# Kernel optimization log

Measured on AMD Instinct MI355X. Metric: run time of the kernel, lower is better.

Reference implementation:

```python
import jax, jax.numpy as jnp
import numpy as np
import math

B, S, D_IN, D_OUT = 2, 2048, 2048, 2048
N_HEADS, N_KV = 32, 8
HEAD_DIM = D_OUT // N_HEADS  # 64
GROUP = N_HEADS // N_KV      # 4


def _rope_tables(seq_len, head_dim, base=10000.0):
    inv_freq = 1.0 / (base ** (jnp.arange(0, head_dim, 2, dtype=jnp.float32) / head_dim))
    angles = jnp.arange(seq_len, dtype=jnp.float32)[:, None] * inv_freq[None, :]  # [S, hd/2]
    angles = jnp.concatenate([angles, angles], axis=-1)  # [S, hd]
    return jnp.cos(angles), jnp.sin(angles)


def setup_inputs() -> dict:
    key = jax.random.key(0)
    kx, kq, kk, kv, ko = jax.random.split(key, 5)
    x = jax.random.normal(kx, (B, S, D_IN), dtype=jnp.float32)
    # causal mask: True where attention is disallowed (j > i)
    mask = jnp.triu(jnp.ones((S, S), dtype=bool), k=1)
    cos, sin = _rope_tables(S, HEAD_DIM)
    scale = 0.02
    Wq = jax.random.normal(kq, (D_IN, D_OUT), dtype=jnp.float32) * scale
    Wk = jax.random.normal(kk, (D_IN, N_KV * HEAD_DIM), dtype=jnp.float32) * scale
    Wv = jax.random.normal(kv, (D_IN, N_KV * HEAD_DIM), dtype=jnp.float32) * scale
    Wo = jax.random.normal(ko, (D_OUT, D_OUT), dtype=jnp.float32) * scale
    return {"x": x, "mask": mask, "cos": cos, "sin": sin,
            "Wq": Wq, "Wk": Wk, "Wv": Wv, "Wo": Wo}


def _apply_rope(t, cos, sin):
    # t: [B, H, S, hd]; cos/sin: [S, hd]
    hd = t.shape[-1]
    t1, t2 = t[..., : hd // 2], t[..., hd // 2:]
    rotated = jnp.concatenate([-t2, t1], axis=-1)
    return t * cos[None, None] + rotated * sin[None, None]


def reference(x, mask, cos, sin, Wq, Wk, Wv, Wo):
    b, s, _ = x.shape
    q = (x @ Wq).reshape(b, s, N_HEADS, HEAD_DIM).transpose(0, 2, 1, 3)  # [B,H,S,hd]
    k = (x @ Wk).reshape(b, s, N_KV, HEAD_DIM).transpose(0, 2, 1, 3)    # [B,G,S,hd]
    v = (x @ Wv).reshape(b, s, N_KV, HEAD_DIM).transpose(0, 2, 1, 3)
    q = _apply_rope(q, cos, sin)
    k = _apply_rope(k, cos, sin)
    # repeat_interleave KV heads to match query heads
    k = jnp.repeat(k, GROUP, axis=1)  # [B,H,S,hd]
    v = jnp.repeat(v, GROUP, axis=1)
    scores = jnp.einsum('bhqd,bhkd->bhqk', q, k)
    scores = jnp.where(mask[None, None], -1e9, scores)
    weights = jax.nn.softmax(scores / math.sqrt(HEAD_DIM), axis=-1)
    ctx = jnp.einsum('bhqk,bhkd->bhqd', weights, v)
    ctx = ctx.transpose(0, 2, 1, 3).reshape(b, s, D_OUT)
    return ctx @ Wo
```

## Files before the change

kernel.cpp:

```cpp
#include <hip/hip_runtime.h>
#include <hip/hip_bf16.h>

using bf16 = __bf16;
using bf16x8 = __attribute__((ext_vector_type(8))) __bf16;
using bf16x4 = __attribute__((ext_vector_type(4))) __bf16;
using f32x4  = __attribute__((ext_vector_type(4))) float;
using f32x16 = __attribute__((ext_vector_type(16))) float;

typedef const void __attribute__((address_space(1)))* gas_p;
typedef void __attribute__((address_space(3)))* las_p;

#define GLD16(g, l) __builtin_amdgcn_global_load_lds((gas_p)(const void*)(g), (las_p)(void*)(l), 16, 0, 0)

__device__ __forceinline__ bf16x8 lds_ld8(const void* p) {
  union { uint4 u; bf16x8 v; } c;
  c.u = *(const uint4*)p;
  return c.v;
}
__device__ __forceinline__ bf16x8 g_ld8(const bf16* p) {
  union { uint4 u; bf16x8 v; } c;
  c.u = *(const uint4*)p;
  return c.v;
}
__device__ __forceinline__ float fexp2(float x) {
  float r; asm("v_exp_f32 %0, %1" : "=v"(r) : "v"(x)); return r;
}
__device__ __forceinline__ unsigned cvtpk(float lo, float hi) {
  unsigned r; asm("v_cvt_pk_bf16_f32 %0, %1, %2" : "=v"(r) : "v"(lo), "v"(hi)); return r;
}

__global__ void k_pre(const float* __restrict__ x, bf16* __restrict__ xb,
                      const float* __restrict__ Wq, const float* __restrict__ Wk,
                      const float* __restrict__ Wv, const float* __restrict__ Wo,
                      bf16* __restrict__ wqkv, bf16* __restrict__ wo_t) {
  const int id = blockIdx.x;
  if (id < 8192) {
    const int i = id * 256 + threadIdx.x;
    float4 f = ((const float4*)x)[i];
    bf16x4 o;
    o[0] = (bf16)f.x; o[1] = (bf16)f.y; o[2] = (bf16)f.z; o[3] = (bf16)f.w;
    ((bf16x4*)xb)[i] = o;
    return;
  }
  __shared__ float tile[64][65];
  const int u0 = id - 8192;
  const float* W; bf16* dst; int N, rowOff, bx, by;
  if (u0 < 1024)      { W = Wq; dst = wqkv; N = 2048; rowOff = 0;    bx = u0 & 31; by = u0 >> 5; }
  else if (u0 < 1280) { int u = u0 - 1024; W = Wk; dst = wqkv; N = 512; rowOff = 2048; bx = u & 7; by = u >> 3; }
  else if (u0 < 1536) { int u = u0 - 1280; W = Wv; dst = wqkv; N = 512; rowOff = 2560; bx = u & 7; by = u >> 3; }
  else                { int u = u0 - 1536; W = Wo; dst = wo_t; N = 2048; rowOff = 0;   bx = u & 31; by = u >> 5; }
  const int n0 = bx * 64, k0 = by * 64;
  const int t = threadIdx.x;
#pragma unroll
  for (int i = 0; i < 16; ++i) {
    int idx = t + i * 256; int r = idx >> 6, c = idx & 63;
    tile[r][c] = W[(size_t)(k0 + r) * N + n0 + c];
  }
  __syncthreads();
#pragma unroll
  for (int i = 0; i < 16; ++i) {
    int idx = t + i * 256; int r = idx >> 6, c = idx & 63;
    dst[(size_t)(rowOff + n0 + r) * 2048 + k0 + c] = (bf16)tile[c][r];
  }
}

__device__ __forceinline__ void gemm_main(const bf16* __restrict__ A, const bf16* __restrict__ Bt,
                                          int brow, int bcol, int tid, f32x4 (&acc)[4][4],
                                          char* ldsA, char* ldsB) {
  const int lane = tid & 63;
  const int l15 = lane & 15, l4 = lane >> 4;
  const int wid = tid >> 6, wr = wid >> 1, wc = wid & 1;
  const int srow = tid >> 3;
  const int xseg = (tid & 7) ^ (srow & 7);
  const bf16* ga = A  + (size_t)(brow + srow) * 2048 + xseg * 8;
  const bf16* gb = Bt + (size_t)(bcol + srow) * 2048 + xseg * 8;
  char* la = ldsA + tid * 16;
  char* lb = ldsB + tid * 16;

  for (int k0 = 0; k0 < 2048; k0 += 64) {
    __syncthreads();
#pragma unroll
    for (int i = 0; i < 4; ++i) {
      GLD16(ga + k0 + (size_t)(32 * i) * 2048, la + i * 4096);
      GLD16(gb + k0 + (size_t)(32 * i) * 2048, lb + i * 4096);
    }
    __syncthreads();
#pragma unroll
    for (int kk = 0; kk < 2; ++kk) {
      bf16x8 af[4], bfr[4];
#pragma unroll
      for (int m = 0; m < 4; ++m) {
        const int row = wr * 64 + m * 16 + l15;
        af[m] = lds_ld8(ldsA + row * 128 + ((kk * 64 + l4 * 16) ^ ((row & 7) << 4)));
      }
#pragma unroll
      for (int n = 0; n < 4; ++n) {
        const int row = wc * 64 + n * 16 + l15;
        bfr[n] = lds_ld8(ldsB + row * 128 + ((kk * 64 + l4 * 16) ^ ((row & 7) << 4)));
      }
#pragma unroll
      for (int m = 0; m < 4; ++m)
#pragma unroll
        for (int n = 0; n < 4; ++n)
          acc[m][n] = __builtin_amdgcn_mfma_f32_16x16x32_bf16(af[m], bfr[n], acc[m][n], 0, 0, 0);
    }
  }
}

__global__ __launch_bounds__(256) void k_gemm_qkv(const bf16* __restrict__ A, const bf16* __restrict__ Bt,
    const float* __restrict__ cosT, const float* __restrict__ sinT,
    bf16* __restrict__ Qb, bf16* __restrict__ Kb, bf16* __restrict__ Vt) {
  __shared__ __align__(16) char ldsA[16384];
  __shared__ __align__(16) char ldsB[16384];
  const int tid = threadIdx.x;
  const int p = (int)blockIdx.x, r8 = p & 7, q8 = p >> 3;
  const int by = r8 * 3 + q8 % 3, bx = q8 / 3;
  const int brow = bx * 128, bcol = by * 128;
  f32x4 zero = {0.f, 0.f, 0.f, 0.f};
  f32x4 acc[4][4];
#pragma unroll
  for (int m = 0; m < 4; ++m)
#pragma unroll
    for (int n = 0; n < 4; ++n) acc[m][n] = zero;

  gemm_main(A, Bt, brow, bcol, tid, acc, ldsA, ldsB);

  const int lane = tid & 63, l15 = lane & 15, l4 = lane >> 4;
  const int wid = tid >> 6, wr = wid >> 1, wc = wid & 1;
  const int base64 = bcol + wc * 64;
  const int rbase  = brow + wr * 64;

  if (base64 < 2048) {
    const int h = base64 >> 6;
#pragma unroll
    for (int m = 0; m < 4; ++m)
#pragma unroll
      for (int r = 0; r < 4; ++r) {
        const int row = rbase + m * 16 + l4 * 4 + r;
        const int b = row >> 11, s = row & 2047;
        float o[4];
#pragma unroll
        for (int n = 0; n < 4; ++n) {
          const int d = n * 16 + l15;
          const float cv = cosT[s * 64 + d], sv = sinT[s * 64 + d];
          const float t = acc[m][n][r], pp = acc[m][n ^ 2][r];
          o[n] = (t * cv + ((n < 2) ? -pp : pp) * sv) * 0.18033688f;
        }
        bf16* dst = Qb + ((size_t)((b * 32 + h) * 2048 + s)) * 64;
#pragma unroll
        for (int n = 0; n < 4; ++n) dst[n * 16 + l15] = (bf16)o[n];
      }
  } else if (base64 < 2560) {
    const int h = (base64 - 2048) >> 6;
#pragma unroll
    for (int m = 0; m < 4; ++m)
#pragma unroll
      for (int r = 0; r < 4; ++r) {
        const int row = rbase + m * 16 + l4 * 4 + r;
        const int b = row >> 11, s = row & 2047;
        float o[4];
#pragma unroll
        for (int n = 0; n < 4; ++n) {
          const int d = n * 16 + l15;
          const float cv = cosT[s * 64 + d], sv = sinT[s * 64 + d];
          const float t = acc[m][n][r], pp = acc[m][n ^ 2][r];
          o[n] = t * cv + ((n < 2) ? -pp : pp) * sv;
        }
        bf16* dst = Kb + ((size_t)((b * 8 + h) * 2048 + s)) * 64;
#pragma unroll
        for (int n = 0; n < 4; ++n) dst[n * 16 + l15] = (bf16)o[n];
      }
  } else {
    const int h = (base64 - 2560) >> 6;
#pragma unroll
    for (int m = 0; m < 4; ++m)
#pragma unroll
      for (int r = 0; r < 4; ++r) {
        const int row = rbase + m * 16 + l4 * 4 + r;
        const int b = row >> 11, s = row & 2047;
        const int ps = (s & ~12) | ((s & 4) << 1) | ((s & 8) >> 1);
#pragma unroll
        for (int n = 0; n < 4; ++n) {
          const int d = n * 16 + l15;
          Vt[((size_t)((b * 8 + h) * 64 + d)) * 2048 + ps] = (bf16)acc[m][n][r];
        }
      }
  }
}

__global__ __launch_bounds__(256) void k_attn(const bf16* __restrict__ Qb, const bf16* __restrict__ Kb,
                                              const bf16* __restrict__ Vtp, bf16* __restrict__ ctx) {
  __shared__ __align__(16) char kvb[3][16384];
  __shared__ __align__(16) char tbuf[4][4096];
  const int tid = threadIdx.x, lane = tid & 63, w = tid >> 6;
  const int l31 = lane & 31, hi = lane >> 5;
  const int p = (int)blockIdx.x;
  const int y = (p & 7) * 8 + ((p >> 3) & 7);
  const int j = p >> 6;
  const int b = y >> 5, h = y & 31, hk = h >> 2;
  int c = 15 - j;
  const int ntA = 2 * c + 2;
  const int NT = 34;
  int q0 = c * 128 + w * 32;
  int nf = (q0 + 31) >> 6;

  const int srow = tid >> 3, sseg = tid & 7;
  const bf16* kS = Kb  + ((size_t)((b * 8 + hk) * 2048)) * 64;
  const bf16* vS = Vtp + ((size_t)((b * 8 + hk) * 64)) * 2048;
  const int sz = (l31 & 7) << 4;
  const int wsz = (srow & 7) << 4;

  const f32x16 z16 = {0,0,0,0,0,0,0,0,0,0,0,0,0,0,0,0};
  f32x16 o[2];
  float m, lsum;
  bf16x8 bq[4];

  auto load_q = [&]() {
    const bf16* qbase = Qb + ((size_t)((b * 32 + h) * 2048 + q0 + l31)) * 64 + hi * 8;
#pragma unroll
    for (int dc = 0; dc < 4; ++dc) bq[dc] = g_ld8(qbase + dc * 16);
  };
  load_q();
  o[0] = z16; o[1] = z16; m = -3.0e38f; lsum = 0.f;

  uint4 st[4];
  auto stage_load = [&](int kv0) {
#pragma unroll
    for (int r4 = 0; r4 < 4; ++r4) {
      const int row = srow + (r4 & 1) * 32;
      const bf16* g = (r4 < 2) ? (kS + (size_t)(kv0 + row) * 64 + sseg * 8)
                               : (vS + (size_t)row * 2048 + kv0 + sseg * 8);
      st[r4] = *(const uint4*)g;
    }
  };
  auto stage_write = [&](char* buf) {
#pragma unroll
    for (int r4 = 0; r4 < 4; ++r4)
      *(uint4*)(buf + (srow + r4 * 32) * 128 + ((sseg * 16) ^ wsz)) = st[r4];
  };

  union PF { unsigned u[4]; bf16x8 v; };
  PF pf[4];
  int pend = 0, pslot = 0;

  auto pv_issue = [&](char* pbuf) {
    __builtin_amdgcn_s_setprio(1);
#pragma unroll
    for (int cc = 0; cc < 4; ++cc)
#pragma unroll
      for (int dh = 0; dh < 2; ++dh) {
        const int row = 64 + dh * 32 + l31;
        bf16x8 av = lds_ld8(pbuf + row * 128 + ((cc * 32 + hi * 16) ^ sz));
        o[dh] = __builtin_amdgcn_mfma_f32_32x32x16_bf16(av, pf[cc].v, o[dh], 0, 0, 0);
      }
    __builtin_amdgcn_s_setprio(0);
  };

  auto epilogue = [&]() {
    float ll = lsum + __shfl_xor(lsum, 32);
    const float inv = 1.0f / ll;
    char* tb = tbuf[w];
#pragma unroll
    for (int dh = 0; dh < 2; ++dh)
#pragma unroll
      for (int r = 0; r < 16; r += 2) {
        const unsigned wdv = cvtpk(o[dh][r] * inv, o[dh][r + 1] * inv);
        const int d = dh * 32 + (r & 3) + 8 * (r >> 2) + 4 * hi;
        *(unsigned*)(tb + l31 * 128 + ((d * 2) ^ sz)) = wdv;
      }
#pragma unroll
    for (int jj = 0; jj < 4; ++jj) {
      const int off = hi * 16 + jj * 32;
      uint4 val = *(const uint4*)(tb + l31 * 128 + (off ^ sz));
      *(uint4*)(ctx + ((size_t)(b * 2048 + q0 + l31)) * 2048 + h * 64 + off / 2) = val;
    }
  };

  stage_load(0);
  stage_write(kvb[0]);
  __syncthreads();

  for (int g = 0; g < NT; ++g) {
    const int kt = (g < ntA) ? g : g - ntA;
    char* cur = kvb[g % 3];
    if (g + 1 < NT) {
      const int gn = g + 1;
      stage_load(((gn < ntA) ? gn : gn - ntA) * 64);
    }
    if (pend) { pv_issue(kvb[pslot]); pend = 0; }
    if (kt <= nf) {
      const int kv0 = kt * 64;
      f32x16 sc[2];
      __builtin_amdgcn_s_setprio(1);
#pragma unroll
      for (int kvh = 0; kvh < 2; ++kvh) {
        const int row = kvh * 32 + l31;
        bf16x8 a0 = lds_ld8(cur + row * 128 + ((hi * 16) ^ sz));
        sc[kvh] = __builtin_amdgcn_mfma_f32_32x32x16_bf16(a0, bq[0], z16, 0, 0, 0);
#pragma unroll
        for (int dc = 1; dc < 4; ++dc) {
          bf16x8 ad = lds_ld8(cur + row * 128 + ((dc * 32 + hi * 16) ^ sz));
          sc[kvh] = __builtin_amdgcn_mfma_f32_32x32x16_bf16(ad, bq[dc], sc[kvh], 0, 0, 0);
        }
      }
      __builtin_amdgcn_s_setprio(0);
      if (kt == nf) {
        const int q = q0 + l31;
#pragma unroll
        for (int kvh = 0; kvh < 2; ++kvh)
#pragma unroll
          for (int r = 0; r < 16; ++r) {
            const int kv = kv0 + kvh * 32 + (r & 3) + 8 * (r >> 2) + 4 * hi;
            if (kv > q) sc[kvh][r] = -3.0e30f;
          }
      }
      float t[16];
#pragma unroll
      for (int i = 0; i < 16; ++i) t[i] = fmaxf(sc[0][i], sc[1][i]);
#pragma unroll
      for (int stp = 8; stp >= 1; stp >>= 1)
#pragma unroll
        for (int i = 0; i < stp; ++i) t[i] = fmaxf(t[i], t[i + stp]);
      float mx = fmaxf(t[0], __shfl_xor(t[0], 32));
      if (!__all(mx <= m + 11.5f)) {
        const float mn = fmaxf(m, mx);
        const float corr = fexp2(m - mn);
        m = mn;
        lsum *= corr;
#pragma unroll
        for (int r = 0; r < 16; ++r) { o[0][r] *= corr; o[1][r] *= corr; }
      }
#pragma unroll
      for (int kvh = 0; kvh < 2; ++kvh)
#pragma unroll
        for (int r = 0; r < 16; ++r) sc[kvh][r] = fexp2(sc[kvh][r] - m);
#pragma unroll
      for (int kvh = 0; kvh < 2; ++kvh)
#pragma unroll
        for (int s = 0; s < 2; ++s)
#pragma unroll
          for (int tt = 0; tt < 4; ++tt)
            pf[kvh * 2 + s].u[tt] = cvtpk(sc[kvh][s * 8 + 2 * tt], sc[kvh][s * 8 + 2 * tt + 1]);
      pend = 1; pslot = g % 3;
      float u[16];
#pragma unroll
      for (int i = 0; i < 16; ++i) u[i] = sc[0][i] + sc[1][i];
#pragma unroll
      for (int stp = 8; stp >= 1; stp >>= 1)
#pragma unroll
        for (int i = 0; i < stp; ++i) u[i] += u[i + stp];
      lsum += u[0];
    }
    if (g + 1 < NT) stage_write(kvb[(g + 1) % 3]);
    __syncthreads();
    if (g == ntA - 1) {
      if (pend) { pv_issue(kvb[pslot]); pend = 0; }
      epilogue();
      c = j; q0 = c * 128 + w * 32; nf = (q0 + 31) >> 6;
      load_q();
      o[0] = z16; o[1] = z16; m = -3.0e38f; lsum = 0.f;
    }
  }
  if (pend) { pv_issue(kvb[pslot]); pend = 0; }
  epilogue();
}

__global__ __launch_bounds__(256) void k_gemm_out(const bf16* __restrict__ A, const bf16* __restrict__ Bt,
                                                  float* __restrict__ out) {
  __shared__ __align__(16) char ldsA[16384];
  __shared__ __align__(16) char ldsB[16384];
  const int tid = threadIdx.x;
  const int p = (int)blockIdx.x, r8 = p & 7, q8 = p >> 3;
  const int by = r8 * 2 + (q8 & 1), bx = q8 >> 1;
  const int brow = bx * 128, bcol = by * 128;
  f32x4 zero = {0.f, 0.f, 0.f, 0.f};
  f32x4 acc[4][4];
#pragma unroll
  for (int m = 0; m < 4; ++m)
#pragma unroll
    for (int n = 0; n < 4; ++n) acc[m][n] = zero;

  gemm_main(A, Bt, brow, bcol, tid, acc, ldsA, ldsB);

  const int lane = tid & 63, l15 = lane & 15, l4 = lane >> 4;
  const int wid = tid >> 6, wr = wid >> 1, wc = wid & 1;
#pragma unroll
  for (int m = 0; m < 4; ++m)
#pragma unroll
    for (int r = 0; r < 4; ++r) {
      const int row = brow + wr * 64 + m * 16 + l4 * 4 + r;
      float* dst = out + (size_t)row * 2048 + bcol + wc * 64;
#pragma unroll
      for (int n = 0; n < 4; ++n) dst[n * 16 + l15] = acc[m][n][r];
    }
}

extern "C" void kernel_launch(void* const* d_in, const int* in_sizes, int n_in,
                              void* d_out, int out_size, void* d_ws, size_t ws_size,
                              hipStream_t stream) {
  (void)in_sizes; (void)n_in; (void)out_size;
  if (ws_size < (size_t)79691776) return;
  const float* x    = (const float*)d_in[0];
  const float* cosT = (const float*)d_in[2];
  const float* sinT = (const float*)d_in[3];
  const float* Wq   = (const float*)d_in[4];
  const float* Wk   = (const float*)d_in[5];
  const float* Wv   = (const float*)d_in[6];
  const float* Wo   = (const float*)d_in[7];
  char* ws = (char*)d_ws;
  bf16* xb   = (bf16*)(ws + 0);
  bf16* wqkv = (bf16*)(ws + 16777216);
  bf16* wo_t = (bf16*)(ws + 29360128);
  bf16* Qb   = (bf16*)(ws + 37748736);
  bf16* Kb   = (bf16*)(ws + 54525952);
  bf16* Vt   = (bf16*)(ws + 58720256);
  bf16* ctxb = (bf16*)(ws + 62914560);
  float* out = (float*)d_out;

  k_pre<<<10752, 256, 0, stream>>>(x, xb, Wq, Wk, Wv, Wo, wqkv, wo_t);
  k_gemm_qkv<<<768, 256, 0, stream>>>(xb, wqkv, cosT, sinT, Qb, Kb, Vt);
  k_attn<<<512, 256, 0, stream>>>(Qb, Kb, Vt, ctxb);
  k_gemm_out<<<512, 256, 0, stream>>>(ctxb, wo_t, out);
}
```

Measured before the change: 217.6 us.

## Process two KV tiles per barrier with double buffering, drop deferred PV

The attention loop now handles two 64-row KV tiles per iteration between barriers, using two 32KB LDS buffers instead of a triple-buffered single-tile ring. This halves the number of __syncthreads calls. The deferred PV MFMA issue, which overlapped the previous tile's PV with the current QK, is replaced by an inline PV right after the softmax of the same tile. The intent is to cut barrier overhead, at the cost of losing the software-pipelined overlap between the softmax and the PV MFMAs, and of using more LDS per block.

Result: no change. 221.7 us (+1.9%).

```diff
diff --git a/kernel.cpp b/kernel.cpp
--- a/kernel.cpp
+++ b/kernel.cpp
@@ -190,7 +190,7 @@
 
 __global__ __launch_bounds__(256) void k_attn(const bf16* __restrict__ Qb, const bf16* __restrict__ Kb,
                                               const bf16* __restrict__ Vtp, bf16* __restrict__ ctx) {
-  __shared__ __align__(16) char kvb[3][16384];
+  __shared__ __align__(16) char kvb[2][32768];
   __shared__ __align__(16) char tbuf[4][4096];
   const int tid = threadIdx.x, lane = tid & 63, w = tid >> 6;
   const int l31 = lane & 31, hi = lane >> 5;
@@ -239,21 +239,79 @@
       *(uint4*)(buf + (srow + r4 * 32) * 128 + ((sseg * 16) ^ wsz)) = st[r4];
   };
 
-  union PF { unsigned u[4]; bf16x8 v; };
-  PF pf[4];
-  int pend = 0, pslot = 0;
-
-  auto pv_issue = [&](char* pbuf) {
+  auto tile_body = [&](int kt, char* cur) {
+    if (kt > nf) return;
+    const int kv0 = kt * 64;
+    f32x16 sc[2];
     __builtin_amdgcn_s_setprio(1);
 #pragma unroll
-    for (int cc = 0; cc < 4; ++cc)
-#pragma unroll
-      for (int dh = 0; dh < 2; ++dh) {
-        const int row = 64 + dh * 32 + l31;
-        bf16x8 av = lds_ld8(pbuf + row * 128 + ((cc * 32 + hi * 16) ^ sz));
-        o[dh] = __builtin_amdgcn_mfma_f32_32x32x16_bf16(av, pf[cc].v, o[dh], 0, 0, 0);
-      }
+    for (int kvh = 0; kvh < 2; ++kvh) {
+      const int row = kvh * 32 + l31;
+      bf16x8 a0 = lds_ld8(cur + row * 128 + ((hi * 16) ^ sz));
+      sc[kvh] = __builtin_amdgcn_mfma_f32_32x32x16_bf16(a0, bq[0], z16, 0, 0, 0);
+#pragma unroll
+      for (int dc = 1; dc < 4; ++dc) {
+        bf16x8 ad = lds_ld8(cur + row * 128 + ((dc * 32 + hi * 16) ^ sz));
+        sc[kvh] = __builtin_amdgcn_mfma_f32_32x32x16_bf16(ad, bq[dc], sc[kvh], 0, 0, 0);
+      }
+    }
     __builtin_amdgcn_s_setprio(0);
+    if (kt == nf) {
+      const int q = q0 + l31;
+#pragma unroll
+      for (int kvh = 0; kvh < 2; ++kvh)
+#pragma unroll
+        for (int r = 0; r < 16; ++r) {
+          const int kv = kv0 + kvh * 32 + (r & 3) + 8 * (r >> 2) + 4 * hi;
+          if (kv > q) sc[kvh][r] = -3.0e30f;
+        }
+    }
+    float t[16];
+#pragma unroll
+    for (int i = 0; i < 16; ++i) t[i] = fmaxf(sc[0][i], sc[1][i]);
+#pragma unroll
+    for (int stp = 8; stp >= 1; stp >>= 1)
+#pragma unroll
+      for (int i = 0; i < stp; ++i) t[i] = fmaxf(t[i], t[i + stp]);
+    float mx = fmaxf(t[0], __shfl_xor(t[0], 32));
+    if (!__all(mx <= m + 11.5f)) {
+      const float mn = fmaxf(m, mx);
+      const float corr = fexp2(m - mn);
+      m = mn;
+      lsum *= corr;
+#pragma unroll
+      for (int r = 0; r < 16; ++r) { o[0][r] *= corr; o[1][r] *= corr; }
+    }
+#pragma unroll
+    for (int kvh = 0; kvh < 2; ++kvh)
+#pragma unroll
+      for (int r = 0; r < 16; ++r) sc[kvh][r] = fexp2(sc[kvh][r] - m);
+#pragma unroll
+    for (int kvh = 0; kvh < 2; ++kvh)
+#pragma unroll
+      for (int s = 0; s < 2; ++s) {
+        union { unsigned u[4]; bf16x8 v; } f;
+#pragma unroll
+        for (int tt = 0; tt < 4; ++tt)
+          f.u[tt] = cvtpk(sc[kvh][s * 8 + 2 * tt], sc[kvh][s * 8 + 2 * tt + 1]);
+        const int cc = kvh * 2 + s;
+        __builtin_amdgcn_s_setprio(1);
+#pragma unroll
+        for (int dh = 0; dh < 2; ++dh) {
+          const int row = 64 + dh * 32 + l31;
+          bf16x8 av = lds_ld8(cur + row * 128 + ((cc * 32 + hi * 16) ^ sz));
+          o[dh] = __builtin_amdgcn_mfma_f32_32x32x16_bf16(av, f.v, o[dh], 0, 0, 0);
+        }
+        __builtin_amdgcn_s_setprio(0);
+      }
+    float u[16];
+#pragma unroll
+    for (int i = 0; i < 16; ++i) u[i] = sc[0][i] + sc[1][i];
+#pragma unroll
+    for (int stp = 8; stp >= 1; stp >>= 1)
+#pragma unroll
+      for (int i = 0; i < stp; ++i) u[i] += u[i + stp];
+    lsum += u[0];
   };
 
   auto epilogue = [&]() {
@@ -276,92 +334,31 @@
     }
   };
 
-  stage_load(0);
-  stage_write(kvb[0]);
+  stage_load(0);  stage_write(kvb[0]);
+  stage_load(64); stage_write(kvb[0] + 16384);
   __syncthreads();
 
-  for (int g = 0; g < NT; ++g) {
-    const int kt = (g < ntA) ? g : g - ntA;
-    char* cur = kvb[g % 3];
-    if (g + 1 < NT) {
-      const int gn = g + 1;
-      stage_load(((gn < ntA) ? gn : gn - ntA) * 64);
-    }
-    if (pend) { pv_issue(kvb[pslot]); pend = 0; }
-    if (kt <= nf) {
-      const int kv0 = kt * 64;
-      f32x16 sc[2];
-      __builtin_amdgcn_s_setprio(1);
-#pragma unroll
-      for (int kvh = 0; kvh < 2; ++kvh) {
-        const int row = kvh * 32 + l31;
-        bf16x8 a0 = lds_ld8(cur + row * 128 + ((hi * 16) ^ sz));
-        sc[kvh] = __builtin_amdgcn_mfma_f32_32x32x16_bf16(a0, bq[0], z16, 0, 0, 0);
-#pragma unroll
-        for (int dc = 1; dc < 4; ++dc) {
-          bf16x8 ad = lds_ld8(cur + row * 128 + ((dc * 32 + hi * 16) ^ sz));
-          sc[kvh] = __builtin_amdgcn_mfma_f32_32x32x16_bf16(ad, bq[dc], sc[kvh], 0, 0, 0);
-        }
-      }
-      __builtin_amdgcn_s_setprio(0);
-      if (kt == nf) {
-        const int q = q0 + l31;
-#pragma unroll
-        for (int kvh = 0; kvh < 2; ++kvh)
-#pragma unroll
-          for (int r = 0; r < 16; ++r) {
-            const int kv = kv0 + kvh * 32 + (r & 3) + 8 * (r >> 2) + 4 * hi;
-            if (kv > q) sc[kvh][r] = -3.0e30f;
-          }
-      }
-      float t[16];
-#pragma unroll
-      for (int i = 0; i < 16; ++i) t[i] = fmaxf(sc[0][i], sc[1][i]);
-#pragma unroll
-      for (int stp = 8; stp >= 1; stp >>= 1)
-#pragma unroll
-        for (int i = 0; i < stp; ++i) t[i] = fmaxf(t[i], t[i + stp]);
-      float mx = fmaxf(t[0], __shfl_xor(t[0], 32));
-      if (!__all(mx <= m + 11.5f)) {
-        const float mn = fmaxf(m, mx);
-        const float corr = fexp2(m - mn);
-        m = mn;
-        lsum *= corr;
-#pragma unroll
-        for (int r = 0; r < 16; ++r) { o[0][r] *= corr; o[1][r] *= corr; }
-      }
-#pragma unroll
-      for (int kvh = 0; kvh < 2; ++kvh)
-#pragma unroll
-        for (int r = 0; r < 16; ++r) sc[kvh][r] = fexp2(sc[kvh][r] - m);
-#pragma unroll
-      for (int kvh = 0; kvh < 2; ++kvh)
-#pragma unroll
-        for (int s = 0; s < 2; ++s)
-#pragma unroll
-          for (int tt = 0; tt < 4; ++tt)
-            pf[kvh * 2 + s].u[tt] = cvtpk(sc[kvh][s * 8 + 2 * tt], sc[kvh][s * 8 + 2 * tt + 1]);
-      pend = 1; pslot = g % 3;
-      float u[16];
-#pragma unroll
-      for (int i = 0; i < 16; ++i) u[i] = sc[0][i] + sc[1][i];
-#pragma unroll
-      for (int stp = 8; stp >= 1; stp >>= 1)
-#pragma unroll
-        for (int i = 0; i < stp; ++i) u[i] += u[i + stp];
-      lsum += u[0];
-    }
-    if (g + 1 < NT) stage_write(kvb[(g + 1) % 3]);
+  const int NI = 17;
+  for (int G = 0; G < NI; ++G) {
+    char* cur = kvb[G & 1];
+    char* nxt = kvb[(G + 1) & 1];
+    const int tA = 2 * G, tB = 2 * G + 1;
+    const int t2 = tA + 2, t3 = tB + 2;
+    const bool ld2 = t2 < NT, ld3 = t3 < NT;
+    if (ld2) stage_load(((t2 < ntA) ? t2 : t2 - ntA) * 64);
+    tile_body((tA < ntA) ? tA : tA - ntA, cur);
+    if (ld2) stage_write(nxt);
+    if (ld3) stage_load(((t3 < ntA) ? t3 : t3 - ntA) * 64);
+    tile_body((tB < ntA) ? tB : tB - ntA, cur + 16384);
+    if (ld3) stage_write(nxt + 16384);
     __syncthreads();
-    if (g == ntA - 1) {
-      if (pend) { pv_issue(kvb[pslot]); pend = 0; }
+    if (tB == ntA - 1) {
       epilogue();
       c = j; q0 = c * 128 + w * 32; nf = (q0 + 31) >> 6;
       load_q();
       o[0] = z16; o[1] = z16; m = -3.0e38f; lsum = 0.f;
     }
   }
-  if (pend) { pv_issue(kvb[pslot]); pend = 0; }
   epilogue();
 }
 
```
